# Performance work log

Hardware: AMD Instinct MI355X
Metric: run time of the kernel (lower is better)

Reference implementation:

```python
import jax, jax.numpy as jnp
import numpy as np

N = 128          # number of samples; P = N*(N-1)/2 = 8128 pairs
D = 8128         # feature dim; must equal P for the module's einsum('ij,ji->i')
EPS = 1e-12

# static pair indices matching the original loop order: for i, for j < i
_II, _JJ = np.tril_indices(N, k=-1)  # each length P = 8128


def setup_inputs() -> dict:
    key = jax.random.key(0)
    k1, k2 = jax.random.split(key)
    S_real = jax.random.normal(k1, (N, D), dtype=jnp.float32)
    S_fake = jax.random.normal(k2, (N, D), dtype=jnp.float32)
    return {"S_real": S_real, "S_fake": S_fake}


def _cosine_loss(real, fake, eps):
    # real, fake: [P, D] with P == D
    norm_real = jnp.linalg.norm(real, axis=1, keepdims=True)
    norm_fake = jnp.linalg.norm(fake, axis=1, keepdims=True)
    mat_real = jnp.maximum(real / norm_real, eps)
    mat_fake = jnp.maximum(fake / norm_fake, eps)
    # einsum('ij,ji->i') then sum == total sum of mat_fake * mat_real.T
    return jnp.einsum('ij,ji->i', mat_fake, mat_real).sum()


def reference(S_real, S_fake):
    # vectorized pairwise differences, same order as the python double loop
    v_real = S_real[_II] - S_real[_JJ]   # [P, D]
    v_fake = S_fake[_II] - S_fake[_JJ]   # [P, D]
    return _cosine_loss(v_real, v_fake, EPS)
```

## Files before the change

kernel.cpp:

```cpp
#include <hip/hip_runtime.h>

#define NS   128
#define D_   8128
#define DP_  8192
#define P_   8128
#define PP   8192
#define EPSV 1e-12f
#define NT   127
#define KSPLIT 64

typedef __attribute__((ext_vector_type(8))) short short8;
typedef __attribute__((ext_vector_type(4))) float f32x4;

static __device__ __forceinline__ unsigned short f32_to_bf16_rne(float f) {
    unsigned int u = __float_as_uint(f);
    return (unsigned short)((u + 0x7fffu + ((u >> 16) & 1u)) >> 16);
}
static __device__ __forceinline__ float bf16_lo(unsigned int u) { return __uint_as_float(u << 16); }
static __device__ __forceinline__ float bf16_hi(unsigned int u) { return __uint_as_float(u & 0xffff0000u); }

__global__ void pad_zero(unsigned short* __restrict__ Sr16, unsigned short* __restrict__ Sf16) {
    int e = blockIdx.x * 256 + threadIdx.x;
    int mtx = e >> 10;
    int rem = e & 1023;
    int row = rem >> 3;
    int c4  = rem & 7;
    unsigned short* dst = (mtx ? Sf16 : Sr16) + (size_t)row * DP_ + D_ + 8 * c4;
    uint4 z; z.x = 0u; z.y = 0u; z.z = 0u; z.w = 0u;
    *(uint4*)dst = z;
}

__global__ void __launch_bounds__(256)
gram_cvt(const float* __restrict__ Sr, const float* __restrict__ Sf,
         unsigned short* __restrict__ Sr16, unsigned short* __restrict__ Sf16,
         float* __restrict__ Gpart) {
    int sl = blockIdx.x;
    int m  = blockIdx.y;
    const float* __restrict__ S = m ? Sf : Sr;
    unsigned short* __restrict__ S16 = m ? Sf16 : Sr16;
    float* __restrict__ out = Gpart + ((size_t)sl * 2 + m) * (NS * NS);

    __shared__ short St[128 * 40];

    int t = threadIdx.x;
    int w = t >> 6, l = t & 63;
    int lr = l & 15;
    int kf = (l >> 4) * 8;

    int ks_begin = sl * 4;
    int ks_end   = (ks_begin + 4 < 254) ? ks_begin + 4 : 254;

    f32x4 acc[2][8];
    #pragma unroll
    for (int fr = 0; fr < 2; ++fr)
        #pragma unroll
        for (int c = 0; c < 8; ++c) acc[fr][c] = (f32x4)0.f;

    for (int ks = ks_begin; ks < ks_end; ++ks) {
        int k0 = ks * 32;
        #pragma unroll
        for (int g4 = 0; g4 < 4; ++g4) {
            int task = t + 256 * g4;
            int row  = task >> 3;
            int g    = task & 7;
            float4 v = *(const float4*)(S + (size_t)row * D_ + k0 + 4 * g);
            ushort4 o;
            o.x = f32_to_bf16_rne(v.x);
            o.y = f32_to_bf16_rne(v.y);
            o.z = f32_to_bf16_rne(v.z);
            o.w = f32_to_bf16_rne(v.w);
            *(ushort4*)&St[row * 40 + 4 * g] = o;
            *(ushort4*)(S16 + (size_t)row * DP_ + k0 + 4 * g) = o;
        }
        __syncthreads();

        short8 a0 = *(const short8*)&St[(w * 32 + lr) * 40 + kf];
        short8 a1 = *(const short8*)&St[(w * 32 + 16 + lr) * 40 + kf];
        #pragma unroll
        for (int c = 0; c < 8; ++c) {
            short8 b = *(const short8*)&St[(c * 16 + lr) * 40 + kf];
            acc[0][c] = __builtin_amdgcn_mfma_f32_16x16x32_bf16(a0, b, acc[0][c], 0, 0, 0);
            acc[1][c] = __builtin_amdgcn_mfma_f32_16x16x32_bf16(a1, b, acc[1][c], 0, 0, 0);
        }
        __syncthreads();
    }

    #pragma unroll
    for (int fr = 0; fr < 2; ++fr) {
        int rbase = w * 32 + fr * 16 + (l >> 4) * 4;
        #pragma unroll
        for (int c = 0; c < 8; ++c) {
            int col = c * 16 + lr;
            #pragma unroll
            for (int r = 0; r < 4; ++r)
                out[(rbase + r) * NS + col] = acc[fr][c][r];
        }
    }
}

__global__ void gram_sum(const float* __restrict__ Gpart, float* __restrict__ G) {
    int idx = blockIdx.x * 256 + threadIdx.x;
    int m = idx >> 14, e = idx & 16383;
    float s = 0.f;
    #pragma unroll 8
    for (int sl = 0; sl < KSPLIT; ++sl)
        s += Gpart[((size_t)sl * 2 + m) * (NS * NS) + e];
    G[idx] = s;
}

__global__ void norm_finish(const float* __restrict__ G,
                            float* __restrict__ inv_nr, float* __restrict__ inv_nf,
                            int* __restrict__ opi, int* __restrict__ opj) {
    int p = blockIdx.x * 256 + threadIdx.x;
    if (p >= PP) return;
    if (p >= P_) {
        inv_nr[p] = 0.f;
        inv_nf[p] = 0.f;
        opi[p] = 0;
        opj[p] = 0;
        return;
    }
    int i = (int)((1.0f + sqrtf(8.0f * (float)p + 1.0f)) * 0.5f);
    while (i * (i - 1) / 2 > p) --i;
    while ((i + 1) * i / 2 <= p) ++i;
    int j = p - i * (i - 1) / 2;

    const float* Gr = G;
    const float* Gf = G + NS * NS;
    float nr2 = Gr[i * NS + i] + Gr[j * NS + j] - 2.f * Gr[i * NS + j];
    float nf2 = Gf[i * NS + i] + Gf[j * NS + j] - 2.f * Gf[i * NS + j];
    inv_nr[p] = rsqrtf(fmaxf(nr2, 1e-30f));
    inv_nf[p] = rsqrtf(fmaxf(nf2, 1e-30f));
    opi[p] = i * DP_;
    opj[p] = j * DP_;
}

__global__ void __launch_bounds__(256, 6)
tile7_kernel(const unsigned short* __restrict__ Sr16, const unsigned short* __restrict__ Sf16,
             const float* __restrict__ inv_nr, const float* __restrict__ inv_nf,
             const int* __restrict__ opi, const int* __restrict__ opj,
             float* __restrict__ partials) {
    __shared__ unsigned short Rt[64 * 136];
    __shared__ int   sIp[128], sJp[128];
    __shared__ float sInvF[128];
    __shared__ float wsum[4];

    int t  = threadIdx.x;
    int p0 = blockIdx.x * 128;
    int q0 = blockIdx.y * 64;

    if (t < 128) {
        int p = p0 + t;
        sIp[t]   = opi[p];
        sJp[t]   = opj[p];
        sInvF[t] = inv_nf[p];
    }

    #pragma unroll
    for (int s = 0; s < 4; ++s) {
        int task = t + 256 * s;
        int q = task >> 4, slot = task & 15;
        int gq = q0 + q;
        int oiq = opi[gq], ojq = opj[gq];
        float invr = inv_nr[gq];
        uint4 ua = *(const uint4*)(Sr16 + oiq + p0 + 8 * slot);
        uint4 ub = *(const uint4*)(Sr16 + ojq + p0 + 8 * slot);
        unsigned int r0 = f32_to_bf16_rne(fmaxf((bf16_lo(ua.x) - bf16_lo(ub.x)) * invr, EPSV));
        unsigned int r1 = f32_to_bf16_rne(fmaxf((bf16_hi(ua.x) - bf16_hi(ub.x)) * invr, EPSV));
        unsigned int r2 = f32_to_bf16_rne(fmaxf((bf16_lo(ua.y) - bf16_lo(ub.y)) * invr, EPSV));
        unsigned int r3 = f32_to_bf16_rne(fmaxf((bf16_hi(ua.y) - bf16_hi(ub.y)) * invr, EPSV));
        unsigned int r4 = f32_to_bf16_rne(fmaxf((bf16_lo(ua.z) - bf16_lo(ub.z)) * invr, EPSV));
        unsigned int r5 = f32_to_bf16_rne(fmaxf((bf16_hi(ua.z) - bf16_hi(ub.z)) * invr, EPSV));
        unsigned int r6 = f32_to_bf16_rne(fmaxf((bf16_lo(ua.w) - bf16_lo(ub.w)) * invr, EPSV));
        unsigned int r7 = f32_to_bf16_rne(fmaxf((bf16_hi(ua.w) - bf16_hi(ub.w)) * invr, EPSV));
        uint4 wv;
        wv.x = r0 | (r1 << 16);
        wv.y = r2 | (r3 << 16);
        wv.z = r4 | (r5 << 16);
        wv.w = r6 | (r7 << 16);
        *(uint4*)&Rt[q * 136 + 8 * slot] = wv;
    }
    __syncthreads();

    int pg = t & 31;
    int qg = t >> 5;
    float fr0[8], fr1[8], fr2[8], fr3[8];
    {
        #define LOAD_F(ARR, R)                                                         \
        {                                                                              \
            int prow = 4 * pg + (R);                                                   \
            int oi = sIp[prow], oj = sJp[prow];                                        \
            float invf = sInvF[prow];                                                  \
            uint4 ua = *(const uint4*)(Sf16 + oi + q0 + 8 * qg);                       \
            uint4 ub = *(const uint4*)(Sf16 + oj + q0 + 8 * qg);                       \
            ARR[0] = fmaxf((bf16_lo(ua.x) - bf16_lo(ub.x)) * invf, EPSV);              \
            ARR[1] = fmaxf((bf16_hi(ua.x) - bf16_hi(ub.x)) * invf, EPSV);              \
            ARR[2] = fmaxf((bf16_lo(ua.y) - bf16_lo(ub.y)) * invf, EPSV);              \
            ARR[3] = fmaxf((bf16_hi(ua.y) - bf16_hi(ub.y)) * invf, EPSV);              \
            ARR[4] = fmaxf((bf16_lo(ua.z) - bf16_lo(ub.z)) * invf, EPSV);              \
            ARR[5] = fmaxf((bf16_hi(ua.z) - bf16_hi(ub.z)) * invf, EPSV);              \
            ARR[6] = fmaxf((bf16_lo(ua.w) - bf16_lo(ub.w)) * invf, EPSV);              \
            ARR[7] = fmaxf((bf16_hi(ua.w) - bf16_hi(ub.w)) * invf, EPSV);              \
        }
        LOAD_F(fr0, 0)
        LOAD_F(fr1, 1)
        LOAD_F(fr2, 2)
        LOAD_F(fr3, 3)
        #undef LOAD_F
    }
    float acc = 0.f;
    #pragma unroll
    for (int k = 0; k < 8; ++k) {
        uint2 rt = *(const uint2*)&Rt[(8 * qg + k) * 136 + 4 * pg];
        acc += fr0[k] * bf16_lo(rt.x) + fr1[k] * bf16_hi(rt.x)
             + fr2[k] * bf16_lo(rt.y) + fr3[k] * bf16_hi(rt.y);
    }

    #pragma unroll
    for (int off = 32; off > 0; off >>= 1) acc += __shfl_down(acc, off, 64);
    if ((t & 63) == 0) wsum[t >> 6] = acc;
    __syncthreads();
    if (t == 0) partials[blockIdx.y * 64 + blockIdx.x] = wsum[0] + wsum[1] + wsum[2] + wsum[3];
}

__global__ void norms_kernel(const float* __restrict__ Sr, const float* __restrict__ Sf,
                             float* __restrict__ inv_nr, float* __restrict__ inv_nf,
                             int* __restrict__ opi, int* __restrict__ opj) {
    int p = blockIdx.x;
    int i = (int)((1.0f + sqrtf(8.0f * (float)p + 1.0f)) * 0.5f);
    while (i * (i - 1) / 2 > p) --i;
    while ((i + 1) * i / 2 <= p) ++i;
    int j = p - i * (i - 1) / 2;

    const float4* ri = (const float4*)(Sr + (size_t)i * D_);
    const float4* rj = (const float4*)(Sr + (size_t)j * D_);
    const float4* fi = (const float4*)(Sf + (size_t)i * D_);
    const float4* fj = (const float4*)(Sf + (size_t)j * D_);

    float sr = 0.f, sf = 0.f;
    for (int d = threadIdx.x; d < D_ / 4; d += 256) {
        float4 a = ri[d], b = rj[d];
        float dx = a.x - b.x, dy = a.y - b.y, dz = a.z - b.z, dw = a.w - b.w;
        sr += dx * dx + dy * dy + dz * dz + dw * dw;
        float4 c2 = fi[d], e = fj[d];
        dx = c2.x - e.x; dy = c2.y - e.y; dz = c2.z - e.z; dw = c2.w - e.w;
        sf += dx * dx + dy * dy + dz * dz + dw * dw;
    }
    #pragma unroll
    for (int off = 32; off > 0; off >>= 1) {
        sr += __shfl_down(sr, off, 64);
        sf += __shfl_down(sf, off, 64);
    }
    __shared__ float wr[4], wf[4];
    int wave = threadIdx.x >> 6;
    if ((threadIdx.x & 63) == 0) { wr[wave] = sr; wf[wave] = sf; }
    __syncthreads();
    if (threadIdx.x == 0) {
        inv_nr[p] = 1.0f / sqrtf(wr[0] + wr[1] + wr[2] + wr[3]);
        inv_nf[p] = 1.0f / sqrtf(wf[0] + wf[1] + wf[2] + wf[3]);
        opi[p] = i * D_;
        opj[p] = j * D_;
    }
}

__global__ void __launch_bounds__(256, 6)
tile3_kernel(const float* __restrict__ Sr, const float* __restrict__ Sf,
             const float* __restrict__ inv_nr, const float* __restrict__ inv_nf,
             const int* __restrict__ opi, const int* __restrict__ opj,
             float* __restrict__ partials) {
    __shared__ float Rt[64][65];
    __shared__ int   sIp[64], sJp[64];
    __shared__ float sInvF[64];
    __shared__ float wsum[4];

    int t  = threadIdx.x;
    int p0 = blockIdx.x * 64, q0 = blockIdx.y * 64;

    if (t < 64) {
        int p = p0 + t;
        sIp[t]   = opi[p];
        sJp[t]   = opj[p];
        sInvF[t] = inv_nf[p];
    }
    {
        int c  = t & 15;
        int qr = t >> 4;
        #pragma unroll
        for (int pass = 0; pass < 4; ++pass) {
            int qq = qr + 16 * pass;
            int q  = q0 + qq;
            int oi = opi[q], oj = opj[q];
            float invr = inv_nr[q];
            const float4 a = *(const float4*)(Sr + oi + p0 + 4 * c);
            const float4 b = *(const float4*)(Sr + oj + p0 + 4 * c);
            Rt[4 * c + 0][qq] = fmaxf((a.x - b.x) * invr, EPSV);
            Rt[4 * c + 1][qq] = fmaxf((a.y - b.y) * invr, EPSV);
            Rt[4 * c + 2][qq] = fmaxf((a.z - b.z) * invr, EPSV);
            Rt[4 * c + 3][qq] = fmaxf((a.w - b.w) * invr, EPSV);
        }
    }
    __syncthreads();

    int qg = t & 15;
    int pg = t >> 4;
    float ax = 0.f, ay = 0.f, az = 0.f, aw = 0.f;
    #pragma unroll
    for (int pp = 0; pp < 4; ++pp) {
        int prow = pg + 16 * pp;
        int oi = sIp[prow], oj = sJp[prow];
        float invf = sInvF[prow];
        const float4 fa = *(const float4*)(Sf + oi + q0 + 4 * qg);
        const float4 fb = *(const float4*)(Sf + oj + q0 + 4 * qg);
        const float4 r  = *(const float4*)&Rt[prow][4 * qg];
        ax += fmaxf((fa.x - fb.x) * invf, EPSV) * r.x;
        ay += fmaxf((fa.y - fb.y) * invf, EPSV) * r.y;
        az += fmaxf((fa.z - fb.z) * invf, EPSV) * r.z;
        aw += fmaxf((fa.w - fb.w) * invf, EPSV) * r.w;
    }
    float acc = (ax + ay) + (az + aw);

    #pragma unroll
    for (int off = 32; off > 0; off >>= 1) acc += __shfl_down(acc, off, 64);
    int w = t >> 6;
    if ((t & 63) == 0) wsum[w] = acc;
    __syncthreads();
    if (t == 0) partials[blockIdx.y * NT + blockIdx.x] = wsum[0] + wsum[1] + wsum[2] + wsum[3];
}

__global__ void reduce_kernel(const float* __restrict__ partials, int n, float* __restrict__ out) {
    float s = 0.f;
    for (int idx = threadIdx.x; idx < n; idx += 1024) s += partials[idx];
    #pragma unroll
    for (int off = 32; off > 0; off >>= 1) s += __shfl_down(s, off, 64);
    __shared__ float wbuf[16];
    int wave = threadIdx.x >> 6;
    if ((threadIdx.x & 63) == 0) wbuf[wave] = s;
    __syncthreads();
    if (threadIdx.x == 0) {
        float tot = 0.f;
        #pragma unroll
        for (int k = 0; k < 16; ++k) tot += wbuf[k];
        out[0] = tot;
    }
}

extern "C" void kernel_launch(void* const* d_in, const int* in_sizes, int n_in,
                              void* d_out, int out_size, void* d_ws, size_t ws_size,
                              hipStream_t stream) {
    const float* Sr = (const float*)d_in[0];
    const float* Sf = (const float*)d_in[1];
    float* out = (float*)d_out;

    char* w = (char*)d_ws;
    unsigned short* Sr16 = (unsigned short*)w;   w += (size_t)NS * DP_ * 2;
    unsigned short* Sf16 = (unsigned short*)w;   w += (size_t)NS * DP_ * 2;
    float* inv_nr = (float*)w;                   w += (size_t)PP * 4;
    float* inv_nf = (float*)w;                   w += (size_t)PP * 4;
    int*   opi    = (int*)w;                     w += (size_t)PP * 4;
    int*   opj    = (int*)w;                     w += (size_t)PP * 4;
    float* tpart  = (float*)w;                   w += (size_t)16384 * 4;
    float* Gpart  = (float*)w;                   w += (size_t)KSPLIT * 2 * NS * NS * 4;
    float* G      = (float*)w;                   w += (size_t)2 * NS * NS * 4;
    size_t need = (size_t)(w - (char*)d_ws);

    if (ws_size >= need) {
        pad_zero<<<8, 256, 0, stream>>>(Sr16, Sf16);
        dim3 gg(KSPLIT, 2);
        gram_cvt<<<gg, 256, 0, stream>>>(Sr, Sf, Sr16, Sf16, Gpart);
        gram_sum<<<128, 256, 0, stream>>>(Gpart, G);
        norm_finish<<<32, 256, 0, stream>>>(G, inv_nr, inv_nf, opi, opj);
        dim3 grid(64, 128);
        tile7_kernel<<<grid, 256, 0, stream>>>(Sr16, Sf16, inv_nr, inv_nf, opi, opj, tpart);
        reduce_kernel<<<1, 1024, 0, stream>>>(tpart, 8192, out);
    } else {
        norms_kernel<<<P_, 256, 0, stream>>>(Sr, Sf, inv_nr, inv_nf, opi, opj);
        dim3 grid(NT, NT);
        tile3_kernel<<<grid, 256, 0, stream>>>(Sr, Sf, inv_nr, inv_nf, opi, opj, tpart);
        reduce_kernel<<<1, 1024, 0, stream>>>(tpart, NT * NT, out);
    }
}
```

Before: 62.45 us.

## Shrink pair tiles to 64x64 with fp32 LDS and fold padding into gram

The pairwise tile kernel now uses 64x64 tiles on a 128x128 grid instead of 128x64 tiles. The real-side tile is kept in fp32 shared memory rather than re-rounded to bf16, and the difference/scale math uses packed two-wide float vectors. The gram kernel is split across 127 K-slices of two steps each, and the zero-padding of the bf16 copies is folded into its last slice, which removes one kernel launch. The trade-offs are less data reuse per tile, twice as many partials to reduce, and more Gram partial traffic through gram_sum.

```diff
diff --git a/kernel.cpp b/kernel.cpp
--- a/kernel.cpp
+++ b/kernel.cpp
@@ -7,10 +7,11 @@
 #define PP   8192
 #define EPSV 1e-12f
 #define NT   127
-#define KSPLIT 64
+#define KSPLIT 127
 
 typedef __attribute__((ext_vector_type(8))) short short8;
 typedef __attribute__((ext_vector_type(4))) float f32x4;
+typedef __attribute__((ext_vector_type(2))) float f32x2;
 
 static __device__ __forceinline__ unsigned short f32_to_bf16_rne(float f) {
     unsigned int u = __float_as_uint(f);
@@ -18,17 +19,6 @@
 }
 static __device__ __forceinline__ float bf16_lo(unsigned int u) { return __uint_as_float(u << 16); }
 static __device__ __forceinline__ float bf16_hi(unsigned int u) { return __uint_as_float(u & 0xffff0000u); }
-
-__global__ void pad_zero(unsigned short* __restrict__ Sr16, unsigned short* __restrict__ Sf16) {
-    int e = blockIdx.x * 256 + threadIdx.x;
-    int mtx = e >> 10;
-    int rem = e & 1023;
-    int row = rem >> 3;
-    int c4  = rem & 7;
-    unsigned short* dst = (mtx ? Sf16 : Sr16) + (size_t)row * DP_ + D_ + 8 * c4;
-    uint4 z; z.x = 0u; z.y = 0u; z.z = 0u; z.w = 0u;
-    *(uint4*)dst = z;
-}
 
 __global__ void __launch_bounds__(256)
 gram_cvt(const float* __restrict__ Sr, const float* __restrict__ Sf,
@@ -47,17 +37,15 @@
     int lr = l & 15;
     int kf = (l >> 4) * 8;
 
-    int ks_begin = sl * 4;
-    int ks_end   = (ks_begin + 4 < 254) ? ks_begin + 4 : 254;
-
     f32x4 acc[2][8];
     #pragma unroll
     for (int fr = 0; fr < 2; ++fr)
         #pragma unroll
         for (int c = 0; c < 8; ++c) acc[fr][c] = (f32x4)0.f;
 
-    for (int ks = ks_begin; ks < ks_end; ++ks) {
-        int k0 = ks * 32;
+    #pragma unroll
+    for (int kk = 0; kk < 2; ++kk) {
+        int k0 = (sl * 2 + kk) * 32;
         #pragma unroll
         for (int g4 = 0; g4 < 4; ++g4) {
             int task = t + 256 * g4;
@@ -85,6 +73,16 @@
         __syncthreads();
     }
 
+    if (sl == KSPLIT - 1) {
+        #pragma unroll
+        for (int g = 0; g < 4; ++g) {
+            int idx = t + 256 * g;
+            int row = idx >> 3, c4 = idx & 7;
+            uint4 z; z.x = 0u; z.y = 0u; z.z = 0u; z.w = 0u;
+            *(uint4*)(S16 + (size_t)row * DP_ + D_ + 8 * c4) = z;
+        }
+    }
+
     #pragma unroll
     for (int fr = 0; fr < 2; ++fr) {
         int rbase = w * 32 + fr * 16 + (l >> 4) * 4;
@@ -136,91 +134,103 @@
 }
 
 __global__ void __launch_bounds__(256, 6)
-tile7_kernel(const unsigned short* __restrict__ Sr16, const unsigned short* __restrict__ Sf16,
+tile8_kernel(const unsigned short* __restrict__ Sr16, const unsigned short* __restrict__ Sf16,
              const float* __restrict__ inv_nr, const float* __restrict__ inv_nf,
              const int* __restrict__ opi, const int* __restrict__ opj,
              float* __restrict__ partials) {
-    __shared__ unsigned short Rt[64 * 136];
-    __shared__ int   sIp[128], sJp[128];
-    __shared__ float sInvF[128];
+    __shared__ float Rl[16 * 260];
+    __shared__ int   sOi[64], sOj[64];
+    __shared__ float sInvF[64];
     __shared__ float wsum[4];
 
     int t  = threadIdx.x;
-    int p0 = blockIdx.x * 128;
+    int p0 = blockIdx.x * 64;
     int q0 = blockIdx.y * 64;
 
-    if (t < 128) {
+    if (t < 64) {
         int p = p0 + t;
-        sIp[t]   = opi[p];
-        sJp[t]   = opj[p];
+        sOi[t]   = opi[p];
+        sOj[t]   = opj[p];
         sInvF[t] = inv_nf[p];
     }
 
     #pragma unroll
-    for (int s = 0; s < 4; ++s) {
+    for (int s = 0; s < 2; ++s) {
         int task = t + 256 * s;
-        int q = task >> 4, slot = task & 15;
+        int q = task >> 3, slot = task & 7;
         int gq = q0 + q;
         int oiq = opi[gq], ojq = opj[gq];
         float invr = inv_nr[gq];
         uint4 ua = *(const uint4*)(Sr16 + oiq + p0 + 8 * slot);
         uint4 ub = *(const uint4*)(Sr16 + ojq + p0 + 8 * slot);
-        unsigned int r0 = f32_to_bf16_rne(fmaxf((bf16_lo(ua.x) - bf16_lo(ub.x)) * invr, EPSV));
-        unsigned int r1 = f32_to_bf16_rne(fmaxf((bf16_hi(ua.x) - bf16_hi(ub.x)) * invr, EPSV));
-        unsigned int r2 = f32_to_bf16_rne(fmaxf((bf16_lo(ua.y) - bf16_lo(ub.y)) * invr, EPSV));
-        unsigned int r3 = f32_to_bf16_rne(fmaxf((bf16_hi(ua.y) - bf16_hi(ub.y)) * invr, EPSV));
-        unsigned int r4 = f32_to_bf16_rne(fmaxf((bf16_lo(ua.z) - bf16_lo(ub.z)) * invr, EPSV));
-        unsigned int r5 = f32_to_bf16_rne(fmaxf((bf16_hi(ua.z) - bf16_hi(ub.z)) * invr, EPSV));
-        unsigned int r6 = f32_to_bf16_rne(fmaxf((bf16_lo(ua.w) - bf16_lo(ub.w)) * invr, EPSV));
-        unsigned int r7 = f32_to_bf16_rne(fmaxf((bf16_hi(ua.w) - bf16_hi(ub.w)) * invr, EPSV));
-        uint4 wv;
-        wv.x = r0 | (r1 << 16);
-        wv.y = r2 | (r3 << 16);
-        wv.z = r4 | (r5 << 16);
-        wv.w = r6 | (r7 << 16);
-        *(uint4*)&Rt[q * 136 + 8 * slot] = wv;
-    }
-    __syncthreads();
-
-    int pg = t & 31;
-    int qg = t >> 5;
-    float fr0[8], fr1[8], fr2[8], fr3[8];
-    {
-        #define LOAD_F(ARR, R)                                                         \
-        {                                                                              \
-            int prow = 4 * pg + (R);                                                   \
-            int oi = sIp[prow], oj = sJp[prow];                                        \
-            float invf = sInvF[prow];                                                  \
-            uint4 ua = *(const uint4*)(Sf16 + oi + q0 + 8 * qg);                       \
-            uint4 ub = *(const uint4*)(Sf16 + oj + q0 + 8 * qg);                       \
-            ARR[0] = fmaxf((bf16_lo(ua.x) - bf16_lo(ub.x)) * invf, EPSV);              \
-            ARR[1] = fmaxf((bf16_hi(ua.x) - bf16_hi(ub.x)) * invf, EPSV);              \
-            ARR[2] = fmaxf((bf16_lo(ua.y) - bf16_lo(ub.y)) * invf, EPSV);              \
-            ARR[3] = fmaxf((bf16_hi(ua.y) - bf16_hi(ub.y)) * invf, EPSV);              \
-            ARR[4] = fmaxf((bf16_lo(ua.z) - bf16_lo(ub.z)) * invf, EPSV);              \
-            ARR[5] = fmaxf((bf16_hi(ua.z) - bf16_hi(ub.z)) * invf, EPSV);              \
-            ARR[6] = fmaxf((bf16_lo(ua.w) - bf16_lo(ub.w)) * invf, EPSV);              \
-            ARR[7] = fmaxf((bf16_hi(ua.w) - bf16_hi(ub.w)) * invf, EPSV);              \
-        }
-        LOAD_F(fr0, 0)
-        LOAD_F(fr1, 1)
-        LOAD_F(fr2, 2)
-        LOAD_F(fr3, 3)
-        #undef LOAD_F
-    }
+        f32x2 inv2; inv2.x = invr; inv2.y = invr;
+        f32x2 A, B, V;
+        f32x4 w0, w1;
+        A.x = bf16_lo(ua.x); A.y = bf16_hi(ua.x);
+        B.x = bf16_lo(ub.x); B.y = bf16_hi(ub.x);
+        V = (A - B) * inv2;
+        w0.x = fmaxf(V.x, EPSV); w0.y = fmaxf(V.y, EPSV);
+        A.x = bf16_lo(ua.y); A.y = bf16_hi(ua.y);
+        B.x = bf16_lo(ub.y); B.y = bf16_hi(ub.y);
+        V = (A - B) * inv2;
+        w0.z = fmaxf(V.x, EPSV); w0.w = fmaxf(V.y, EPSV);
+        A.x = bf16_lo(ua.z); A.y = bf16_hi(ua.z);
+        B.x = bf16_lo(ub.z); B.y = bf16_hi(ub.z);
+        V = (A - B) * inv2;
+        w1.x = fmaxf(V.x, EPSV); w1.y = fmaxf(V.y, EPSV);
+        A.x = bf16_lo(ua.w); A.y = bf16_hi(ua.w);
+        B.x = bf16_lo(ub.w); B.y = bf16_hi(ub.w);
+        V = (A - B) * inv2;
+        w1.z = fmaxf(V.x, EPSV); w1.w = fmaxf(V.y, EPSV);
+        float* dst = &Rl[(q >> 2) * 260 + (q & 3) * 64 + 8 * slot];
+        *(f32x4*)dst = w0;
+        *(f32x4*)(dst + 4) = w1;
+    }
+    __syncthreads();
+
+    int qg = t & 15;
+    int pg = t >> 4;
+    int4   oi4 = *(const int4*)&sOi[4 * pg];
+    int4   oj4 = *(const int4*)&sOj[4 * pg];
+    float4 if4 = *(const float4*)&sInvF[4 * pg];
+    int oiA[4] = {oi4.x, oi4.y, oi4.z, oi4.w};
+    int ojA[4] = {oj4.x, oj4.y, oj4.z, oj4.w};
+    float ifA[4] = {if4.x, if4.y, if4.z, if4.w};
+
+    f32x2 F[4][2];
+    #pragma unroll
+    for (int r = 0; r < 4; ++r) {
+        uint2 ua = *(const uint2*)(Sf16 + oiA[r] + q0 + 4 * qg);
+        uint2 ub = *(const uint2*)(Sf16 + ojA[r] + q0 + 4 * qg);
+        f32x2 inv2; inv2.x = ifA[r]; inv2.y = ifA[r];
+        f32x2 A0, A1, B0, B1;
+        A0.x = bf16_lo(ua.x); A0.y = bf16_hi(ua.x);
+        A1.x = bf16_lo(ua.y); A1.y = bf16_hi(ua.y);
+        B0.x = bf16_lo(ub.x); B0.y = bf16_hi(ub.x);
+        B1.x = bf16_lo(ub.y); B1.y = bf16_hi(ub.y);
+        f32x2 V0 = (A0 - B0) * inv2;
+        f32x2 V1 = (A1 - B1) * inv2;
+        F[r][0].x = fmaxf(V0.x, EPSV); F[r][0].y = fmaxf(V0.y, EPSV);
+        F[r][1].x = fmaxf(V1.x, EPSV); F[r][1].y = fmaxf(V1.y, EPSV);
+    }
+
     float acc = 0.f;
-    #pragma unroll
-    for (int k = 0; k < 8; ++k) {
-        uint2 rt = *(const uint2*)&Rt[(8 * qg + k) * 136 + 4 * pg];
-        acc += fr0[k] * bf16_lo(rt.x) + fr1[k] * bf16_hi(rt.x)
-             + fr2[k] * bf16_lo(rt.y) + fr3[k] * bf16_hi(rt.y);
+    const float* rbase = &Rl[qg * 260 + 4 * pg];
+    #pragma unroll
+    for (int k = 0; k < 4; ++k) {
+        f32x4 Rv = *(const f32x4*)(rbase + k * 64);
+        float fq0 = (k & 1) ? F[0][k >> 1].y : F[0][k >> 1].x;
+        float fq1 = (k & 1) ? F[1][k >> 1].y : F[1][k >> 1].x;
+        float fq2 = (k & 1) ? F[2][k >> 1].y : F[2][k >> 1].x;
+        float fq3 = (k & 1) ? F[3][k >> 1].y : F[3][k >> 1].x;
+        acc += fq0 * Rv.x + fq1 * Rv.y + fq2 * Rv.z + fq3 * Rv.w;
     }
 
     #pragma unroll
     for (int off = 32; off > 0; off >>= 1) acc += __shfl_down(acc, off, 64);
     if ((t & 63) == 0) wsum[t >> 6] = acc;
     __syncthreads();
-    if (t == 0) partials[blockIdx.y * 64 + blockIdx.x] = wsum[0] + wsum[1] + wsum[2] + wsum[3];
+    if (t == 0) partials[blockIdx.y * 128 + blockIdx.x] = wsum[0] + wsum[1] + wsum[2] + wsum[3];
 }
 
 __global__ void norms_kernel(const float* __restrict__ Sr, const float* __restrict__ Sf,
@@ -364,14 +374,13 @@
     size_t need = (size_t)(w - (char*)d_ws);
 
     if (ws_size >= need) {
-        pad_zero<<<8, 256, 0, stream>>>(Sr16, Sf16);
         dim3 gg(KSPLIT, 2);
         gram_cvt<<<gg, 256, 0, stream>>>(Sr, Sf, Sr16, Sf16, Gpart);
         gram_sum<<<128, 256, 0, stream>>>(Gpart, G);
         norm_finish<<<32, 256, 0, stream>>>(G, inv_nr, inv_nf, opi, opj);
-        dim3 grid(64, 128);
-        tile7_kernel<<<grid, 256, 0, stream>>>(Sr16, Sf16, inv_nr, inv_nf, opi, opj, tpart);
-        reduce_kernel<<<1, 1024, 0, stream>>>(tpart, 8192, out);
+        dim3 grid(128, 128);
+        tile8_kernel<<<grid, 256, 0, stream>>>(Sr16, Sf16, inv_nr, inv_nf, opi, opj, tpart);
+        reduce_kernel<<<1, 1024, 0, stream>>>(tpart, 16384, out);
     } else {
         norms_kernel<<<P_, 256, 0, stream>>>(Sr, Sf, inv_nr, inv_nf, opi, opj);
         dim3 grid(NT, NT);
```

New measurement: 62.86 us. Within noise of the previous version (+0.7%).
